# Kernel tuning notes

Hardware: AMD Instinct MI355X
Metric: run time of the kernel (lower is better)

The kernel has to match this reference:

```python
import jax, jax.numpy as jnp
import numpy as np

E = 2        # expan_att_chans
HEADS = 16   # num_chans * expan_att_chans


def _gconv1x1(x, w, b, groups):
    # Grouped 1x1 conv. x: [B, Cin, H, W]; w: [Cout, Cin//groups]; b: [Cout].
    # Output channel layout matches torch: group-major (c_group * gout + o).
    B, Cin, H, W = x.shape
    Cout = w.shape[0]
    gin, gout = Cin // groups, Cout // groups
    y = jnp.einsum('bgip,goi->bgop',
                   x.reshape(B, groups, gin, H * W),
                   w.reshape(groups, gout, gin))
    return y.reshape(B, Cout, H, W) + b[None, :, None, None]


def _l2norm(x, eps=1e-12):
    # F.normalize(dim=-1): x / max(||x||_2, eps)
    n = jnp.sqrt(jnp.sum(x * x, axis=-1, keepdims=True))
    return x / jnp.maximum(n, eps)


def setup_inputs() -> dict:
    key = jax.random.key(0)
    ks = jax.random.split(key, 12)
    B, C, H, W = 8, 128, 128, 128
    s = 0.05  # small init (module uses xavier gain=0.01)
    f32 = jnp.float32
    return {
        'x': jax.random.normal(ks[0], (B, C, H, W), f32),
        'to': jax.random.normal(ks[1], (B, C, H, W), f32),
        't': jnp.ones((1, HEADS, 1, 1), f32),
        # rgb qkv chain (fusion): C -> 2EC -> EC -> EC, all groups=C
        'w_r1': (jax.random.normal(ks[2], (C * E * 2, 1), f32) * s),
        'b_r1': jnp.zeros((C * E * 2,), f32),
        'w_r2': (jax.random.normal(ks[3], (C * E, 2 * E), f32) * s),
        'b_r2': jnp.zeros((C * E,), f32),
        'w_r3': (jax.random.normal(ks[4], (C * E, E), f32) * s),
        'b_r3': jnp.zeros((C * E,), f32),
        # text kv chain: C -> 2EC -> EC -> 2EC, all groups=C
        'w_t1': (jax.random.normal(ks[5], (C * E * 2, 1), f32) * s),
        'b_t1': jnp.zeros((C * E * 2,), f32),
        'w_t2': (jax.random.normal(ks[6], (C * E, 2 * E), f32) * s),
        'b_t2': jnp.zeros((C * E,), f32),
        'w_t3': (jax.random.normal(ks[7], (C * E * 2, E), f32) * s),
        'b_t3': jnp.zeros((C * E * 2,), f32),
        # fusion conv: Conv2d(E*C -> C, k=3, stride=1, pad=1) + LeakyReLU(0.2)
        'w_f': (jax.random.normal(ks[8], (C, C * E, 3, 3), f32) * 0.02),
        'b_f': jnp.zeros((C,), f32),
    }


def reference(x, to, t, w_r1, b_r1, w_r2, b_r2, w_r3, b_r3,
              w_t1, b_t1, w_t2, b_t2, w_t3, b_t3, w_f, b_f):
    B, C, H, W = x.shape
    Cexp = E * C
    d = Cexp // HEADS  # per-head channel dim
    HW = H * W

    # grouped 1x1 conv chains producing Q (from rgb) and K,V (from text)
    q = _gconv1x1(_gconv1x1(_gconv1x1(x, w_r1, b_r1, C), w_r2, b_r2, C), w_r3, b_r3, C)      # [B, EC, H, W]
    kv = _gconv1x1(_gconv1x1(_gconv1x1(to, w_t1, b_t1, C), w_t2, b_t2, C), w_t3, b_t3, C)    # [B, 2EC, H, W]

    # Rearrange 'B (C E) H W -> B E C H W' then view as [B, heads, d, HW]
    q = q.reshape(B, C, E, HW).transpose(0, 2, 1, 3).reshape(B, HEADS, d, HW)
    kv = kv.reshape(B, C, 2 * E, HW).transpose(0, 2, 1, 3)  # [B, 2E, C, HW]
    k = kv[:, :E].reshape(B, HEADS, d, HW)
    v = kv[:, E:].reshape(B, HEADS, d, HW)

    # channel (transposed) attention with L2-normalized Q,K and learned temperature
    qn, kn = _l2norm(q), _l2norm(k)
    attn = jax.nn.softmax(jnp.einsum('bhdp,bhep->bhde', qn, kn) * t, axis=-1)  # [B, H, d, d]
    xo = jnp.einsum('bhde,bhep->bhdp', attn, v)  # [B, heads, d, HW]

    # rearrange 'B C X (H W) -> B (X C) H W' with C=heads, X=d  (d-major, head-minor)
    xo = xo.transpose(0, 2, 1, 3).reshape(B, Cexp, H, W)

    # group_fus: 3x3 conv (stride 1, pad 1) + LeakyReLU(0.2), residual add
    y = jax.lax.conv_general_dilated(
        xo, w_f, window_strides=(1, 1), padding=((1, 1), (1, 1)),
        dimension_numbers=('NCHW', 'OIHW', 'NCHW'))
    y = jax.nn.leaky_relu(y + b_f[None, :, None, None], negative_slope=0.2)
    return x + y
```

## Files before the change

kernel.cpp:

```cpp
#include <hip/hip_runtime.h>
#include <math.h>

#define B_  8
#define C_  128
#define H_  128
#define W_  128
#define HW_ 16384

#define OFF_MPART 0
#define OFF_SPART 262144
#define OFF_M     327680
#define OFF_S     344064
#define OFF_WV    348160
#define OFF_CST   380928
#define OFF_T     382976
#define OFF_WEFF  392192
#define OFF_T2F   982016
#define T2_ROW    16640
#define T2_BATCH  2163200
#define WS_NEED   (982016ull * 4ull + 34611200ull)

typedef __attribute__((ext_vector_type(8))) short short8;
typedef __attribute__((ext_vector_type(4))) float f32x4;

__device__ __forceinline__ unsigned short f2bf(float f) {
  unsigned u = __float_as_uint(f);
  u += 0x7fffu + ((u >> 16) & 1u);
  return (unsigned short)(u >> 16);
}

__device__ __forceinline__ f32x4 mfma16(short8 a, short8 b, f32x4 c) {
  return __builtin_amdgcn_mfma_f32_16x16x32_bf16(a, b, c, 0, 0, 0);
}

__device__ __forceinline__ void gl16(const void* g, void* l) {
  const unsigned loff = (unsigned)(unsigned long long)l;
  __builtin_amdgcn_global_load_lds(
      (const __attribute__((address_space(1))) void*)g,
      (__attribute__((address_space(3))) void*)loff, 16, 0, 0);
}

__device__ __forceinline__ float wave_sum64(float v) {
  v += __shfl_xor(v, 1);
  v += __shfl_xor(v, 2);
  v += __shfl_xor(v, 4);
  v += __shfl_xor(v, 8);
  v += __shfl_xor(v, 16);
  v += __shfl_xor(v, 32);
  return v;
}

__global__ __launch_bounds__(256) void k_reduce(const float* __restrict__ x,
                                                const float* __restrict__ to,
                                                float* __restrict__ ws) {
  const int bid  = blockIdx.x;
  const int kc   = bid & 7;
  const int blk  = (bid >> 3) & 7;
  const int b    = bid >> 6;
  const int wave = threadIdx.x >> 6;
  const int lane = threadIdx.x & 63;
  const int c0   = blk * 16;
  const int i0   = wave * 4;

  const f32x4* xb4 = (const f32x4*)(x  + ((size_t)b * C_ + c0) * HW_);
  const f32x4* tb4 = (const f32x4*)(to + ((size_t)b * C_ + c0) * HW_);

  float acc[4][16];
#pragma unroll
  for (int a = 0; a < 4; ++a)
#pragma unroll
    for (int j = 0; j < 16; ++j) acc[a][j] = 0.f;
  float sx[4] = {0,0,0,0}, sxx[4] = {0,0,0,0}, st[4] = {0,0,0,0}, stt[4] = {0,0,0,0};

  const int pbase4 = kc * 512 + lane;
#pragma unroll 1
  for (int it = 0; it < 8; ++it) {
    const int p4 = pbase4 + it * 64;
    f32x4 tv[16];
#pragma unroll
    for (int j = 0; j < 16; ++j) tv[j] = tb4[(size_t)j * 4096 + p4];
    f32x4 xv[4];
#pragma unroll
    for (int a = 0; a < 4; ++a) xv[a] = xb4[(size_t)(i0 + a) * 4096 + p4];
#pragma unroll
    for (int a = 0; a < 4; ++a) {
      const f32x4 xa = xv[a];
#pragma unroll
      for (int j = 0; j < 16; ++j) {
        const f32x4 tj = tv[j];
        float s = acc[a][j];
        s = fmaf(xa[0], tj[0], s);
        s = fmaf(xa[1], tj[1], s);
        s = fmaf(xa[2], tj[2], s);
        s = fmaf(xa[3], tj[3], s);
        acc[a][j] = s;
      }
      sx[a] += xa[0] + xa[1] + xa[2] + xa[3];
      float q = sxx[a];
      q = fmaf(xa[0], xa[0], q); q = fmaf(xa[1], xa[1], q);
      q = fmaf(xa[2], xa[2], q); q = fmaf(xa[3], xa[3], q);
      sxx[a] = q;
    }
#pragma unroll
    for (int j = 0; j < 16; ++j)
      if ((j >> 2) == wave) {
        const f32x4 tj = tv[j];
        st[j & 3] += tj[0] + tj[1] + tj[2] + tj[3];
        float q = stt[j & 3];
        q = fmaf(tj[0], tj[0], q); q = fmaf(tj[1], tj[1], q);
        q = fmaf(tj[2], tj[2], q); q = fmaf(tj[3], tj[3], q);
        stt[j & 3] = q;
      }
  }

#pragma unroll
  for (int a = 0; a < 4; ++a) {
#pragma unroll
    for (int j = 0; j < 16; ++j) acc[a][j] = wave_sum64(acc[a][j]);
    sx[a]  = wave_sum64(sx[a]);
    sxx[a] = wave_sum64(sxx[a]);
    st[a]  = wave_sum64(st[a]);
    stt[a] = wave_sum64(stt[a]);
  }

  if (lane == 0) {
    float* Mp = ws + OFF_MPART + (size_t)((b * 8 + blk) * 16 + kc) * 256;
#pragma unroll
    for (int a = 0; a < 4; ++a)
#pragma unroll
      for (int j = 0; j < 16; ++j) Mp[(i0 + a) * 16 + j] = acc[a][j];
    float* Sp = ws + OFF_SPART;
#pragma unroll
    for (int a = 0; a < 4; ++a) {
      const int cidx = b * C_ + c0 + i0 + a;
      Sp[0 * 16384 + cidx * 16 + kc] = sx[a];
      Sp[1 * 16384 + cidx * 16 + kc] = sxx[a];
      Sp[2 * 16384 + cidx * 16 + kc] = st[a];
      Sp[3 * 16384 + cidx * 16 + kc] = stt[a];
    }
  }
}

__global__ __launch_bounds__(256) void k_redB(float* __restrict__ ws) {
  const int gid = blockIdx.x * 256 + threadIdx.x;
  if (gid < 16384) {
    const float* mp = ws + OFF_MPART + (size_t)(gid >> 8) * 4096 + (gid & 255);
    float s = 0.f;
#pragma unroll
    for (int kc = 0; kc < 8; ++kc) s += mp[kc * 256];
    ws[OFF_M + gid] = s;
  } else {
    const int sidx = gid - 16384;
    const float* sp = ws + OFF_SPART + (size_t)sidx * 16;
    float s = 0.f;
#pragma unroll
    for (int kc = 0; kc < 8; ++kc) s += sp[kc];
    ws[OFF_S + sidx] = s;
  }
}

__global__ __launch_bounds__(256) void k_zero(unsigned short* __restrict__ t2) {
  const int b = blockIdx.x >> 1, r = blockIdx.x & 1;
  unsigned short* row = t2 + (size_t)b * T2_BATCH + (size_t)(r ? 129 : 0) * T2_ROW;
  const short8 z = {0,0,0,0,0,0,0,0};
  for (int idx = threadIdx.x; idx < 2080; idx += 256)
    *(short8*)(row + (size_t)idx * 8) = z;
}

__global__ __launch_bounds__(256) void k_tr(const float* __restrict__ to,
                                            unsigned short* __restrict__ t2) {
  const int d  = blockIdx.x;
  const int xh = d & 1;
  const int y  = (d >> 1) & 127;
  const int b  = d >> 8;
  const int tid = threadIdx.x;
  __shared__ char lds[64 * 256];

  const int x0 = xh * 64;
  const int xq = tid & 15;
  const int cg = tid >> 4;
  const float* srcb = to + ((size_t)b * C_ + cg * 8) * HW_ + (size_t)y * W_ + x0 + xq * 4;
#pragma unroll
  for (int k = 0; k < 8; ++k) {
    const f32x4 v = *(const f32x4*)(srcb + (size_t)k * HW_);
    const int c = cg * 8 + k;
#pragma unroll
    for (int e = 0; e < 4; ++e) {
      const int xl = xq * 4 + e;
      const int boff = xl * 256 + ((2 * c) ^ ((xl & 7) << 4));
      *(unsigned short*)(lds + boff) = f2bf(v[e]);
    }
  }
  __syncthreads();

  unsigned short* rowbase = t2 + (size_t)b * T2_BATCH + (size_t)(y + 1) * T2_ROW;
#pragma unroll
  for (int i = 0; i < 4; ++i) {
    const int xx = tid >> 2;
    const int cs = (tid & 3) + i * 4;
    short8 val = *(short8*)(lds + xx * 256 + ((cs * 16) ^ ((xx & 7) << 4)));
    *(short8*)(rowbase + (size_t)(x0 + xx + 1) * 128 + cs * 8) = val;
  }
  if (tid < 16) {
    short8 z = {0,0,0,0,0,0,0,0};
    if (xh == 0) *(short8*)(rowbase + tid * 8) = z;
    else         *(short8*)(rowbase + (size_t)129 * 128 + tid * 8) = z;
  }
}

__global__ __launch_bounds__(256) void k_attn(const float* __restrict__ t,
    const float* __restrict__ w_r1, const float* __restrict__ b_r1,
    const float* __restrict__ w_r2, const float* __restrict__ b_r2,
    const float* __restrict__ w_r3, const float* __restrict__ b_r3,
    const float* __restrict__ w_t1, const float* __restrict__ b_t1,
    const float* __restrict__ w_t2, const float* __restrict__ b_t2,
    const float* __restrict__ w_t3, const float* __restrict__ b_t3,
    float* __restrict__ ws) {
  const int b = blockIdx.x;
  const int tid = threadIdx.x;
  __shared__ float aQ[256], bQ[256], aK[256], bK[256], aV[256], bV[256];
  __shared__ float rks[256], kAs[256], kBs[256], stos[256];

  if (tid < 128) {
    const int g = tid;
    float A1[4], B1[4], A2[2], B2[2];
#pragma unroll
    for (int j = 0; j < 4; ++j) { A1[j] = w_r1[g * 4 + j]; B1[j] = b_r1[g * 4 + j]; }
#pragma unroll
    for (int i = 0; i < 2; ++i) {
      A2[i] = 0.f; B2[i] = b_r2[g * 2 + i];
#pragma unroll
      for (int j = 0; j < 4; ++j) {
        const float w = w_r2[(g * 2 + i) * 4 + j];
        A2[i] = fmaf(w, A1[j], A2[i]); B2[i] = fmaf(w, B1[j], B2[i]);
      }
    }
#pragma unroll
    for (int o = 0; o < 2; ++o) {
      float a = 0.f, bb = b_r3[g * 2 + o];
#pragma unroll
      for (int i = 0; i < 2; ++i) {
        const float w = w_r3[(g * 2 + o) * 2 + i];
        a = fmaf(w, A2[i], a); bb = fmaf(w, B2[i], bb);
      }
      aQ[g * 2 + o] = a; bQ[g * 2 + o] = bb;
    }
#pragma unroll
    for (int j = 0; j < 4; ++j) { A1[j] = w_t1[g * 4 + j]; B1[j] = b_t1[g * 4 + j]; }
#pragma unroll
    for (int i = 0; i < 2; ++i) {
      A2[i] = 0.f; B2[i] = b_t2[g * 2 + i];
#pragma unroll
      for (int j = 0; j < 4; ++j) {
        const float w = w_t2[(g * 2 + i) * 4 + j];
        A2[i] = fmaf(w, A1[j], A2[i]); B2[i] = fmaf(w, B1[j], B2[i]);
      }
    }
#pragma unroll
    for (int o = 0; o < 4; ++o) {
      float a = 0.f, bb = b_t3[g * 4 + o];
#pragma unroll
      for (int i = 0; i < 2; ++i) {
        const float w = w_t3[(g * 4 + o) * 2 + i];
        a = fmaf(w, A2[i], a); bb = fmaf(w, B2[i], bb);
      }
      if (o < 2) { aK[g * 2 + o] = a; bK[g * 2 + o] = bb; }
      else       { aV[g * 2 + (o - 2)] = a; bV[g * 2 + (o - 2)] = bb; }
    }
  }
  __syncthreads();

  const float* S   = ws + OFF_S;
  const float* Sx  = S;
  const float* Sxx = S + 1024;
  const float* Sto = S + 2048;
  const float* Stt = S + 3072;

  {
    const int h = tid >> 4, e = h >> 3, blk = h & 7, c0 = blk * 16;
    const int g = c0 + (tid & 15);
    const float a = aK[g * 2 + e], bb = bK[g * 2 + e];
    const float s2 = a * a * Stt[b * C_ + g] + 2.f * a * bb * Sto[b * C_ + g]
                   + bb * bb * 16384.f;
    rks[tid] = 1.f / fmaxf(sqrtf(fmaxf(s2, 0.f)), 1e-12f);
    kAs[tid] = a; kBs[tid] = bb;
    stos[tid] = Sto[b * C_ + g];
  }
  __syncthreads();

  {
    const int h = tid >> 4, i = tid & 15, e = h >> 3, blk = h & 7, c0 = blk * 16;
    const int gi = c0 + i;
    const float gA = aQ[gi * 2 + e], gB = bQ[gi * 2 + e];
    const float sxi = Sx[b * C_ + gi];
    const float q2 = gA * gA * Sxx[b * C_ + gi] + 2.f * gA * gB * sxi
                   + gB * gB * 16384.f;
    const float rnq = 1.f / fmaxf(sqrtf(fmaxf(q2, 0.f)), 1e-12f);
    const float tt = t[h];
    const float* Mrow = ws + OFF_M + (size_t)(b * 8 + blk) * 256 + i * 16;

    float lg[16];
    float mx = -1e30f;
#pragma unroll
    for (int j = 0; j < 16; ++j) {
      const float s = gA * kAs[h * 16 + j] * Mrow[j]
                    + gA * kBs[h * 16 + j] * sxi
                    + gB * kAs[h * 16 + j] * stos[h * 16 + j]
                    + gB * kBs[h * 16 + j] * 16384.f;
      const float l = tt * s * rnq * rks[h * 16 + j];
      lg[j] = l;
      mx = fmaxf(mx, l);
    }
    float den = 0.f;
#pragma unroll
    for (int j = 0; j < 16; ++j) { const float ev = expf(lg[j] - mx); lg[j] = ev; den += ev; }
    const float inv = 1.f / den;
    float cs = 0.f;
    float* WVp = ws + OFF_WV + (size_t)(b * 16 + h) * 256 + i * 16;
#pragma unroll
    for (int j = 0; j < 16; ++j) {
      const float aa = lg[j] * inv;
      const int gj = c0 + j;
      WVp[j] = aa * aV[gj * 2 + e];
      cs = fmaf(aa, bV[gj * 2 + e], cs);
    }
    ws[OFF_CST + b * 256 + i * 16 + h] = cs;
  }
}

__global__ __launch_bounds__(128) void k_weff(const float* __restrict__ w_f,
                                              float* __restrict__ ws) {
  const int b = blockIdx.x >> 7, oc = blockIdx.x & 127;
  const int c = threadIdx.x, blk = c >> 4, j = c & 15;
  const float* WVb = ws + OFF_WV;
  float acc[9];
#pragma unroll
  for (int k = 0; k < 9; ++k) acc[k] = 0.f;
#pragma unroll
  for (int e = 0; e < 2; ++e) {
    const int h = e * 8 + blk;
#pragma unroll
    for (int i = 0; i < 16; ++i) {
      const float coef = WVb[((size_t)(b * 16 + h) * 16 + i) * 16 + j];
      const float* wf = w_f + (size_t)(oc * 256 + i * 16 + h) * 9;
#pragma unroll
      for (int k = 0; k < 9; ++k) acc[k] = fmaf(wf[k], coef, acc[k]);
    }
  }
  unsigned short* wb16 = (unsigned short*)(ws + OFF_WEFF);
#pragma unroll
  for (int k = 0; k < 9; ++k)
    wb16[(((size_t)(b * 9 + k)) * 128 + oc) * 128 + c] = f2bf(acc[k]);

  __shared__ float tp[9][128];
  float tl[9];
#pragma unroll
  for (int k = 0; k < 9; ++k) tl[k] = 0.f;
  const float* cst = ws + OFF_CST + b * 256;
  for (int cc = c; cc < 256; cc += 128) {
    const float cv = cst[cc];
    const float* wf = w_f + (size_t)(oc * 256 + cc) * 9;
#pragma unroll
    for (int k = 0; k < 9; ++k) tl[k] = fmaf(wf[k], cv, tl[k]);
  }
#pragma unroll
  for (int k = 0; k < 9; ++k) tp[k][c] = tl[k];
  __syncthreads();
  for (int s = 64; s > 0; s >>= 1) {
    if (c < s) {
#pragma unroll
      for (int k = 0; k < 9; ++k) tp[k][c] += tp[k][c + s];
    }
    __syncthreads();
  }
  if (c < 9) ws[OFF_T + ((size_t)b * 128 + oc) * 9 + c] = tp[c][0];
}

__global__ __launch_bounds__(512, 4) void k_conv(const float* __restrict__ xin,
                                                 const float* __restrict__ b_f,
                                                 const float* __restrict__ ws,
                                                 const unsigned short* __restrict__ t2,
                                                 float* __restrict__ out) {
  const int d = blockIdx.x;
  const int b = d & 7;
  const int y = d >> 3;
  const int tid = threadIdx.x;

  __shared__ unsigned short As[2][128 * 64];
  __shared__ unsigned short Bs[2][128 * 64];

  const unsigned short* wb = (const unsigned short*)(ws + OFF_WEFF)
      + (size_t)b * 9 * 16384;
  const unsigned short* t2y = t2 + (size_t)b * T2_BATCH + (size_t)y * T2_ROW;

  const int l = tid & 63;
  const int lm = l & 15, lh = l >> 4;
  const int wv = tid >> 6;
  const int oc0w = (wv >> 1) * 32;
  const int px0w = (wv & 1) * 64;

  const int trow0 = tid >> 3, tci0 = tid & 7;
  const unsigned udst0 = (unsigned)((tid & ~63) * 16);
  const unsigned udst1 = udst0 + 512u * 16u;

#define STAGE(BUF, S)                                                          \
  {                                                                            \
    const int tap_ = (S) >> 1, ks_ = (S) & 1;                                  \
    const int dy_ = tap_ / 3, dx_ = tap_ - dy_ * 3;                            \
    const unsigned short* asrc = wb + (size_t)tap_ * 16384 + ks_ * 64;         \
    const unsigned short* bsrc = t2y + (size_t)dy_ * T2_ROW + dx_ * 128 + ks_ * 64; \
    gl16(asrc + (size_t)trow0 * 128 + ((tci0 ^ (trow0 & 7)) << 3),             \
         (char*)&As[BUF][0] + udst0);                                          \
    gl16(asrc + (size_t)(trow0 + 64) * 128 + ((tci0 ^ ((trow0 + 64) & 7)) << 3), \
         (char*)&As[BUF][0] + udst1);                                          \
    gl16(bsrc + (size_t)trow0 * 128 + ((tci0 ^ (trow0 & 7)) << 3),             \
         (char*)&Bs[BUF][0] + udst0);                                          \
    gl16(bsrc + (size_t)(trow0 + 64) * 128 + ((tci0 ^ ((trow0 + 64) & 7)) << 3), \
         (char*)&Bs[BUF][0] + udst1);                                          \
  }

  f32x4 acc[2][4];
#pragma unroll
  for (int mt = 0; mt < 2; ++mt)
#pragma unroll
    for (int nt = 0; nt < 4; ++nt) acc[mt][nt] = (f32x4)0.f;

  STAGE(0, 0);
  __syncthreads();

  int cur = 0;
#pragma unroll 1
  for (int s = 0; s < 18; ++s) {
    if (s + 1 < 18) STAGE(cur ^ 1, s + 1);

    const char* Ab = (const char*)&As[cur][0];
    const char* Bb = (const char*)&Bs[cur][0];
#pragma unroll
    for (int ki = 0; ki < 2; ++ki) {
      short8 af[2], bfr[4];
#pragma unroll
      for (int mt = 0; mt < 2; ++mt) {
        const int oc = oc0w + mt * 16 + lm;
        af[mt] = *(const short8*)(Ab + oc * 128 + (((ki * 4 + lh) ^ (oc & 7)) << 4));
      }
#pragma unroll
      for (int nt = 0; nt < 4; ++nt) {
        const int px = px0w + nt * 16 + lm;
        bfr[nt] = *(const short8*)(Bb + px * 128 + (((ki * 4 + lh) ^ (px & 7)) << 4));
      }
#pragma unroll
      for (int mt = 0; mt < 2; ++mt) {
        acc[mt][0] = mfma16(af[mt], bfr[0], acc[mt][0]);
        acc[mt][1] = mfma16(af[mt], bfr[1], acc[mt][1]);
        acc[mt][2] = mfma16(af[mt], bfr[2], acc[mt][2]);
        acc[mt][3] = mfma16(af[mt], bfr[3], acc[mt][3]);
      }
    }
    __syncthreads();
    cur ^= 1;
  }
#undef STAGE

  float* sm = (float*)&As[0][0];
  if (tid < 128) {
    const float* Tk = ws + OFF_T + (size_t)(b * 128 + tid) * 9;
    float s = Tk[3] + Tk[4] + Tk[5], sl = Tk[3], sr = Tk[5];
    if (y >= 1)   { s += Tk[0] + Tk[1] + Tk[2]; sl += Tk[0]; sr += Tk[2]; }
    if (y <= 126) { s += Tk[6] + Tk[7] + Tk[8]; sl += Tk[6]; sr += Tk[8]; }
    sm[tid] = s + b_f[tid]; sm[128 + tid] = sl; sm[256 + tid] = sr;
  }
  __syncthreads();

#pragma unroll
  for (int mt = 0; mt < 2; ++mt)
#pragma unroll
    for (int nt = 0; nt < 4; ++nt) {
      const int px = px0w + nt * 16 + lm;
#pragma unroll
      for (int r = 0; r < 4; ++r) {
        const int oc = oc0w + mt * 16 + lh * 4 + r;
        float add = sm[oc];
        if (px == 0)   add -= sm[128 + oc];
        if (px == 127) add -= sm[256 + oc];
        const float z = acc[mt][nt][r] + add;
        const size_t base = ((size_t)(b * C_ + oc)) * HW_ + (size_t)y * W_ + px;
        const float rx = xin[base];
        out[base] = rx + (z >= 0.f ? z : 0.2f * z);
      }
    }
}

__global__ __launch_bounds__(512, 4) void k_conv_fb(const float* __restrict__ xin,
                                                    const float* __restrict__ to,
                                                    const float* __restrict__ b_f,
                                                    const float* __restrict__ ws,
                                                    float* __restrict__ out) {
  const int bid = blockIdx.x;
  const int nb  = (bid & 7) * 128 + (bid >> 3);
  const int b   = nb >> 7;
  const int y   = nb & 127;
  const int tid = threadIdx.x;

  __shared__ f32x4 ldsbuf[3120];
  char* lp = (char*)ldsbuf;

  f32x4 acc[4][2];
#pragma unroll
  for (int mt = 0; mt < 4; ++mt)
#pragma unroll
    for (int nt = 0; nt < 2; ++nt) acc[mt][nt] = (f32x4)0.f;

  const float* tob = to + (size_t)b * C_ * HW_;
  const unsigned short* wb16 =
      (const unsigned short*)(ws + OFF_WEFF) + (size_t)b * 9 * 128 * 128;

  const int l = tid & 63, wv = tid >> 6;
  const int ocb0 = (wv & 1) * 64, pxb0 = (wv >> 1) * 32;
  const int lm = l & 15, lh = l >> 4;

  for (int cb = 0; cb < 128; cb += 64) {
    __syncthreads();
    {
      const int xg = tid & 31, cq = (tid >> 5) & 15;
      const int cbase = cb + cq * 4;
#pragma unroll
      for (int row = 0; row < 3; ++row) {
        const int y_in = y + row - 1;
        const bool yok = ((unsigned)y_in < 128u);
        const float* src = tob + (size_t)cbase * HW_ + (size_t)y_in * W_;
#pragma unroll
        for (int xb = 0; xb < 5; ++xb) {
          const int xi = xb * 32 + xg;
          if (xi < 130) {
            const int x_in = xi - 1;
            const bool ok = yok && ((unsigned)x_in < 128u);
            float f0 = 0.f, f1 = 0.f, f2 = 0.f, f3 = 0.f;
            if (ok) {
              f0 = src[x_in];
              f1 = src[HW_ + x_in];
              f2 = src[2 * HW_ + x_in];
              f3 = src[3 * HW_ + x_in];
            }
            ushort4 pk;
            pk.x = f2bf(f0); pk.y = f2bf(f1); pk.z = f2bf(f2); pk.w = f2bf(f3);
            const int boff = (row * 130 + xi) * 128 + ((cq * 8) ^ ((xi & 7) << 4));
            *(ushort4*)(lp + boff) = pk;
          }
        }
      }
    }
    __syncthreads();

    for (int tap = 0; tap < 9; ++tap) {
      const int dy = tap / 3, dx = tap - dy * 3;
#pragma unroll
      for (int ks = 0; ks < 2; ++ks) {
        short8 bfr[2];
#pragma unroll
        for (int nt = 0; nt < 2; ++nt) {
          const int xi = pxb0 + nt * 16 + lm + dx;
          const int boff = (dy * 130 + xi) * 128 + ((ks * 64 + lh * 16) ^ ((xi & 7) << 4));
          bfr[nt] = *(const short8*)(lp + boff);
        }
        const int cin = cb + ks * 32 + lh * 8;
#pragma unroll
        for (int mt = 0; mt < 4; ++mt) {
          const int oc = ocb0 + mt * 16 + lm;
          const short8 af = *(const short8*)(wb16 + ((size_t)tap * 128 + oc) * 128 + cin);
          acc[mt][0] = mfma16(af, bfr[0], acc[mt][0]);
          acc[mt][1] = mfma16(af, bfr[1], acc[mt][1]);
        }
      }
    }
  }

  __syncthreads();
  float* sAdd = (float*)ldsbuf;
  float* sLft = sAdd + 128;
  float* sRgt = sAdd + 256;
  if (tid < 128) {
    const float* Tk = ws + OFF_T + (size_t)(b * 128 + tid) * 9;
    float s = Tk[3] + Tk[4] + Tk[5], sl = Tk[3], sr = Tk[5];
    if (y >= 1)   { s += Tk[0] + Tk[1] + Tk[2]; sl += Tk[0]; sr += Tk[2]; }
    if (y <= 126) { s += Tk[6] + Tk[7] + Tk[8]; sl += Tk[6]; sr += Tk[8]; }
    sAdd[tid] = s + b_f[tid]; sLft[tid] = sl; sRgt[tid] = sr;
  }
  __syncthreads();

#pragma unroll
  for (int mt = 0; mt < 4; ++mt)
#pragma unroll
    for (int nt = 0; nt < 2; ++nt) {
      const int px = pxb0 + nt * 16 + lm;
#pragma unroll
      for (int r = 0; r < 4; ++r) {
        const int oc = ocb0 + mt * 16 + lh * 4 + r;
        float add = sAdd[oc];
        if (px == 0)   add -= sLft[oc];
        if (px == 127) add -= sRgt[oc];
        const float z = acc[mt][nt][r] + add;
        const size_t base = ((size_t)(b * C_ + oc)) * HW_ + (size_t)y * W_ + px;
        const float rx = xin[base];
        out[base] = rx + (z >= 0.f ? z : 0.2f * z);
      }
    }
}

extern "C" void kernel_launch(void* const* d_in, const int* in_sizes, int n_in,
                              void* d_out, int out_size, void* d_ws, size_t ws_size,
                              hipStream_t stream) {
  (void)in_sizes; (void)n_in; (void)out_size;
  const float* x    = (const float*)d_in[0];
  const float* to   = (const float*)d_in[1];
  const float* t    = (const float*)d_in[2];
  const float* w_r1 = (const float*)d_in[3];
  const float* b_r1 = (const float*)d_in[4];
  const float* w_r2 = (const float*)d_in[5];
  const float* b_r2 = (const float*)d_in[6];
  const float* w_r3 = (const float*)d_in[7];
  const float* b_r3 = (const float*)d_in[8];
  const float* w_t1 = (const float*)d_in[9];
  const float* b_t1 = (const float*)d_in[10];
  const float* w_t2 = (const float*)d_in[11];
  const float* b_t2 = (const float*)d_in[12];
  const float* w_t3 = (const float*)d_in[13];
  const float* b_t3 = (const float*)d_in[14];
  const float* w_f  = (const float*)d_in[15];
  const float* b_f  = (const float*)d_in[16];
  float* ws  = (float*)d_ws;
  float* out = (float*)d_out;
  unsigned short* t2 = (unsigned short*)(ws + OFF_T2F);
  const bool fast = (ws_size >= WS_NEED);

  k_reduce<<<512, 256, 0, stream>>>(x, to, ws);
  k_redB<<<80, 256, 0, stream>>>(ws);
  if (fast) {
    k_zero<<<16, 256, 0, stream>>>(t2);
    k_tr<<<2048, 256, 0, stream>>>(to, t2);
  }
  k_attn<<<8, 256, 0, stream>>>(t, w_r1, b_r1, w_r2, b_r2, w_r3, b_r3,
                                w_t1, b_t1, w_t2, b_t2, w_t3, b_t3, ws);
  k_weff<<<1024, 128, 0, stream>>>(w_f, ws);
  if (fast) k_conv<<<1024, 512, 0, stream>>>(x, b_f, ws, t2, out);
  else      k_conv_fb<<<1024, 512, 0, stream>>>(x, to, b_f, ws, out);
}
```

Before: 120.1 us.

## Stage a full 3x3 tap per K-step in conv GEMM and merge barriers

The implicit-GEMM conv kernel now loads a whole 128-deep K slice (one tap) per stage instead of two 64-deep halves. This halves the main loop from 18 to 9 iterations, with a 16-way XOR swizzle on the wider LDS rows. The two __syncthreads per iteration become a single explicit vmcnt wait plus barrier at the top of the loop, cutting synchronisation overhead. In exchange, double-buffered LDS grows to 128 KB per block and launch bounds drop to 2, which likely leaves only one block per CU and less latency hiding.

```diff
diff --git a/kernel.cpp b/kernel.cpp
--- a/kernel.cpp
+++ b/kernel.cpp
@@ -376,7 +376,7 @@
   if (c < 9) ws[OFF_T + ((size_t)b * 128 + oc) * 9 + c] = tp[c][0];
 }
 
-__global__ __launch_bounds__(512, 4) void k_conv(const float* __restrict__ xin,
+__global__ __launch_bounds__(512, 2) void k_conv(const float* __restrict__ xin,
                                                  const float* __restrict__ b_f,
                                                  const float* __restrict__ ws,
                                                  const unsigned short* __restrict__ t2,
@@ -386,8 +386,8 @@
   const int y = d >> 3;
   const int tid = threadIdx.x;
 
-  __shared__ unsigned short As[2][128 * 64];
-  __shared__ unsigned short Bs[2][128 * 64];
+  __shared__ unsigned short As[2][128 * 128];
+  __shared__ unsigned short Bs[2][128 * 128];
 
   const unsigned short* wb = (const unsigned short*)(ws + OFF_WEFF)
       + (size_t)b * 9 * 16384;
@@ -399,24 +399,23 @@
   const int oc0w = (wv >> 1) * 32;
   const int px0w = (wv & 1) * 64;
 
-  const int trow0 = tid >> 3, tci0 = tid & 7;
-  const unsigned udst0 = (unsigned)((tid & ~63) * 16);
-  const unsigned udst1 = udst0 + 512u * 16u;
-
-#define STAGE(BUF, S)                                                          \
+  const unsigned udstw = (unsigned)((tid & ~63) * 16);
+
+#define STAGE(BUF, TAP)                                                        \
   {                                                                            \
-    const int tap_ = (S) >> 1, ks_ = (S) & 1;                                  \
-    const int dy_ = tap_ / 3, dx_ = tap_ - dy_ * 3;                            \
-    const unsigned short* asrc = wb + (size_t)tap_ * 16384 + ks_ * 64;         \
-    const unsigned short* bsrc = t2y + (size_t)dy_ * T2_ROW + dx_ * 128 + ks_ * 64; \
-    gl16(asrc + (size_t)trow0 * 128 + ((tci0 ^ (trow0 & 7)) << 3),             \
-         (char*)&As[BUF][0] + udst0);                                          \
-    gl16(asrc + (size_t)(trow0 + 64) * 128 + ((tci0 ^ ((trow0 + 64) & 7)) << 3), \
-         (char*)&As[BUF][0] + udst1);                                          \
-    gl16(bsrc + (size_t)trow0 * 128 + ((tci0 ^ (trow0 & 7)) << 3),             \
-         (char*)&Bs[BUF][0] + udst0);                                          \
-    gl16(bsrc + (size_t)(trow0 + 64) * 128 + ((tci0 ^ ((trow0 + 64) & 7)) << 3), \
-         (char*)&Bs[BUF][0] + udst1);                                          \
+    const int dy_ = (TAP) / 3, dx_ = (TAP) - dy_ * 3;                          \
+    const unsigned short* asrc = wb + (size_t)(TAP) * 16384;                   \
+    const unsigned short* bsrc = t2y + (size_t)dy_ * T2_ROW + dx_ * 128;       \
+    _Pragma("unroll")                                                          \
+    for (int k_ = 0; k_ < 4; ++k_) {                                           \
+      const int task = k_ * 512 + tid;                                         \
+      const int row_ = task >> 4, q_ = task & 15;                              \
+      const int sw_ = (q_ ^ (row_ & 15)) * 8;                                  \
+      gl16(asrc + (size_t)row_ * 128 + sw_,                                    \
+           (char*)&As[BUF][0] + (unsigned)(k_ * 8192) + udstw);                \
+      gl16(bsrc + (size_t)row_ * 128 + sw_,                                    \
+           (char*)&Bs[BUF][0] + (unsigned)(k_ * 8192) + udstw);                \
+    }                                                                          \
   }
 
   f32x4 acc[2][4];
@@ -426,27 +425,29 @@
     for (int nt = 0; nt < 4; ++nt) acc[mt][nt] = (f32x4)0.f;
 
   STAGE(0, 0);
-  __syncthreads();
 
   int cur = 0;
 #pragma unroll 1
-  for (int s = 0; s < 18; ++s) {
-    if (s + 1 < 18) STAGE(cur ^ 1, s + 1);
+  for (int s = 0; s < 9; ++s) {
+    asm volatile("s_waitcnt vmcnt(0)" ::: "memory");
+    __builtin_amdgcn_s_barrier();
+    __builtin_amdgcn_sched_barrier(0);
+    if (s + 1 < 9) STAGE(cur ^ 1, s + 1);
 
     const char* Ab = (const char*)&As[cur][0];
     const char* Bb = (const char*)&Bs[cur][0];
 #pragma unroll
-    for (int ki = 0; ki < 2; ++ki) {
+    for (int ki = 0; ki < 4; ++ki) {
       short8 af[2], bfr[4];
 #pragma unroll
       for (int mt = 0; mt < 2; ++mt) {
         const int oc = oc0w + mt * 16 + lm;
-        af[mt] = *(const short8*)(Ab + oc * 128 + (((ki * 4 + lh) ^ (oc & 7)) << 4));
+        af[mt] = *(const short8*)(Ab + oc * 256 + (((ki * 4 + lh) ^ (oc & 15)) << 4));
       }
 #pragma unroll
       for (int nt = 0; nt < 4; ++nt) {
         const int px = px0w + nt * 16 + lm;
-        bfr[nt] = *(const short8*)(Bb + px * 128 + (((ki * 4 + lh) ^ (px & 7)) << 4));
+        bfr[nt] = *(const short8*)(Bb + px * 256 + (((ki * 4 + lh) ^ (px & 15)) << 4));
       }
 #pragma unroll
       for (int mt = 0; mt < 2; ++mt) {
@@ -456,11 +457,11 @@
         acc[mt][3] = mfma16(af[mt], bfr[3], acc[mt][3]);
       }
     }
-    __syncthreads();
     cur ^= 1;
   }
 #undef STAGE
 
+  __syncthreads();
   float* sm = (float*)&As[0][0];
   if (tid < 128) {
     const float* Tk = ws + OFF_T + (size_t)(b * 128 + tid) * 9;
```

Result: slower. 132.8 us (+10.5%).
